# Optimization experiments

Measured on AMD Instinct MI355X. Metric: run time of the kernel, lower is better.

The kernel has to match this reference:

```python
import jax, jax.numpy as jnp
import numpy as np

N_NODES = 50000
N_EDGES = 800000
IN_CH = 128
OUT_CH = 64


def setup_inputs() -> dict:
    key = jax.random.key(0)
    ks = jax.random.split(key, 8)
    cat = IN_CH + OUT_CH
    scale = 1.0 / np.sqrt(cat)
    return {
        "x": jax.random.normal(ks[0], (N_NODES, IN_CH), dtype=jnp.float32),
        "edge_index": jax.random.randint(ks[1], (2, N_EDGES), 0, N_NODES, dtype=jnp.int64),
        "edge_weight": jax.random.uniform(ks[2], (N_EDGES,), dtype=jnp.float32),
        "hidden_state": jax.random.normal(ks[3], (N_NODES, OUT_CH), dtype=jnp.float32),
        "W_z": jax.random.normal(ks[4], (cat, OUT_CH), dtype=jnp.float32) * scale,
        "b_z": jnp.zeros((OUT_CH,), dtype=jnp.float32),
        "W_r": jax.random.normal(ks[5], (cat, OUT_CH), dtype=jnp.float32) * scale,
        "b_r": jnp.zeros((OUT_CH,), dtype=jnp.float32),
        "W_h": jax.random.normal(ks[6], (cat, OUT_CH), dtype=jnp.float32) * scale,
        "b_h": jnp.zeros((OUT_CH,), dtype=jnp.float32),
    }


def _gcn_norm(row, col, w, num_nodes):
    # PyG GCNConv normalization with self-loops (fill_value=1):
    # norm_e = deg[row]^-1/2 * w_e * deg[col]^-1/2 over loop-augmented edges
    loops = jnp.arange(num_nodes, dtype=row.dtype)
    row = jnp.concatenate([row, loops])
    col = jnp.concatenate([col, loops])
    w = jnp.concatenate([w, jnp.ones((num_nodes,), dtype=w.dtype)])
    deg = jax.ops.segment_sum(w, col, num_segments=num_nodes)
    dinv = jnp.where(deg > 0, jax.lax.rsqrt(deg), 0.0)
    norm = dinv[row] * w * dinv[col]
    return row, col, norm


def _gcn_conv(x_cat, W, b, row, col, norm, num_nodes):
    h = x_cat @ W                                   # (N, out)
    msg = h[row] * norm[:, None]                    # (E+N, out) gather + scale
    out = jax.ops.segment_sum(msg, col, num_segments=num_nodes)
    return out + b


def reference(x, edge_index, edge_weight, hidden_state,
              W_z, b_z, W_r, b_r, W_h, b_h):
    n = x.shape[0]
    row, col, norm = _gcn_norm(edge_index[0], edge_index[1], edge_weight, n)
    xh = jnp.concatenate([x, hidden_state], axis=1)
    z = jax.nn.sigmoid(_gcn_conv(xh, W_z, b_z, row, col, norm, n))
    r = jax.nn.sigmoid(_gcn_conv(xh, W_r, b_r, row, col, norm, n))
    xrh = jnp.concatenate([x, r * hidden_state], axis=1)
    h_cand = jnp.tanh(_gcn_conv(xrh, W_h, b_h, row, col, norm, n))
    return z * hidden_state + (1.0 - z) * h_cand
```

## Files before the change

### kernel.cpp

```cpp
#include <hip/hip_runtime.h>
#include <hip/hip_bf16.h>
#include <cstdint>
#include <cstddef>

#define IN_CH   128
#define OUT_CH  64
#define CAT_CH  192

typedef short bf16x8 __attribute__((ext_vector_type(8)));
typedef float f32x4  __attribute__((ext_vector_type(4)));
typedef unsigned long long u64;
typedef unsigned int u32;

__device__ __forceinline__ float sigmoidf_(float x) { return 1.f / (1.f + __expf(-x)); }

__device__ __forceinline__ unsigned short f2bf(float f) {
    u32 u = __float_as_uint(f);
    u32 r = (u + 0x7fffu + ((u >> 16) & 1u)) >> 16;
    return (unsigned short)r;
}
__device__ __forceinline__ float bflo(u32 v) { return __uint_as_float(v << 16); }
__device__ __forceinline__ float bfhi(u32 v) { return __uint_as_float(v & 0xffff0000u); }
__device__ __forceinline__ float bf1(unsigned short v) { return __uint_as_float((u32)v << 16); }

__global__ void detect_kernel(const unsigned int* __restrict__ ei, int* __restrict__ flag) {
    unsigned int v = ei[(threadIdx.x << 1) + 1];
    unsigned long long b = __ballot(v != 0u);
    if (threadIdx.x == 0) *flag = (b != 0ull) ? 1 : 0;
}

__device__ __forceinline__ int load_col(const void* ei, int i, int E, int f) {
    return f ? ((const int*)ei)[E + i] : (int)((const long long*)ei)[E + i];
}
__device__ __forceinline__ int load_row(const void* ei, int i, int E, int f) {
    return f ? ((const int*)ei)[i] : (int)((const long long*)ei)[i];
}

__global__ void hist2_kernel(const void* __restrict__ ei, const float* __restrict__ w,
                             u64* __restrict__ packed, u32* __restrict__ rank,
                             const int* __restrict__ flag, int E) {
    int i0 = (blockIdx.x * blockDim.x + threadIdx.x) * 4;
    if (i0 >= E) return;
    int f = *flag;
    u32 rk[4];
#pragma unroll
    for (int k = 0; k < 4; k++) {
        int i = i0 + k;
        if (i < E) {
            int c = load_col(ei, i, E, f);
            u32 wq = __float2uint_rn(w[i] * 1048576.0f);
            u64 old = atomicAdd(&packed[c], (1ull << 32) | (u64)wq);
            rk[k] = (u32)(old >> 32);
        }
    }
#pragma unroll
    for (int k = 0; k < 4; k++)
        if (i0 + k < E) rank[i0 + k] = rk[k];
}

__global__ void dinvc_kernel(const u64* __restrict__ packed, float* __restrict__ dinv,
                             int* __restrict__ counts, int n) {
    int i = blockIdx.x * blockDim.x + threadIdx.x;
    if (i >= n) return;
    u64 p = packed[i];
    float wsum = (float)(u32)(p & 0xffffffffull) * (1.0f / 1048576.0f);
    dinv[i] = rsqrtf(1.0f + wsum);
    counts[i] = (int)(p >> 32);
}

__global__ __launch_bounds__(256) void scan1_kernel(const int* __restrict__ counts,
                                                    int* __restrict__ starts,
                                                    int* __restrict__ bsum, int n) {
    __shared__ int s[256];
    int i = blockIdx.x * 256 + threadIdx.x;
    int v = (i < n) ? counts[i] : 0;
    s[threadIdx.x] = v;
    __syncthreads();
#pragma unroll
    for (int d = 1; d < 256; d <<= 1) {
        int t = (threadIdx.x >= d) ? s[threadIdx.x - d] : 0;
        __syncthreads();
        s[threadIdx.x] += t;
        __syncthreads();
    }
    if (i < n) starts[i] = s[threadIdx.x] - v;
    if (threadIdx.x == 255) bsum[blockIdx.x] = s[255];
}

__global__ __launch_bounds__(256) void scan2_kernel(int* __restrict__ bsum, int nb) {
    __shared__ int s[256];
    int t = threadIdx.x;
    int v = (t < nb) ? bsum[t] : 0;
    s[t] = v;
    __syncthreads();
#pragma unroll
    for (int d = 1; d < 256; d <<= 1) {
        int u = (t >= d) ? s[t - d] : 0;
        __syncthreads();
        s[t] += u;
        __syncthreads();
    }
    if (t < nb) bsum[t] = s[t] - v;
}

__global__ void scan3_kernel(int* __restrict__ starts, const int* __restrict__ boff,
                             int n, int E) {
    int i = blockIdx.x * blockDim.x + threadIdx.x;
    if (i == 0) starts[n] = E;
    if (i < n) starts[i] += boff[blockIdx.x];
}

__global__ void scatter2_kernel(const void* __restrict__ ei, const float* __restrict__ w,
                                const float* __restrict__ dinv, const int* __restrict__ starts,
                                const u32* __restrict__ rank, u64* __restrict__ pairs,
                                const int* __restrict__ flag, int E) {
    int i0 = (blockIdx.x * blockDim.x + threadIdx.x) * 4;
    if (i0 >= E) return;
    int f = *flag;
    int r[4], c[4];
#pragma unroll
    for (int k = 0; k < 4; k++) {
        int i = i0 + k;
        if (i < E) { r[k] = load_row(ei, i, E, f); c[k] = load_col(ei, i, E, f); }
    }
#pragma unroll
    for (int k = 0; k < 4; k++) {
        int i = i0 + k;
        if (i < E) {
            float nm = dinv[r[k]] * w[i] * dinv[c[k]];
            int pos = starts[c[k]] + (int)rank[i];
            pairs[pos] = ((u64)__float_as_uint(nm) << 32) | (u32)r[k];
        }
    }
}

__global__ void cvt_kernel(const float* __restrict__ x, const float* __restrict__ hidden,
                           unsigned short* __restrict__ xb, unsigned short* __restrict__ hb,
                           int nx, int nh) {
    int i4 = (blockIdx.x * blockDim.x + threadIdx.x) * 4;
    if (i4 < nx) {
        float4 v = *(const float4*)&x[i4];
        ushort4 o = { f2bf(v.x), f2bf(v.y), f2bf(v.z), f2bf(v.w) };
        *(ushort4*)&xb[i4] = o;
    } else {
        int j = i4 - nx;
        if (j < nh) {
            float4 v = *(const float4*)&hidden[j];
            ushort4 o = { f2bf(v.x), f2bf(v.y), f2bf(v.z), f2bf(v.w) };
            *(ushort4*)&hb[j] = o;
        }
    }
}

__global__ void packW_kernel(const float* __restrict__ Wz, const float* __restrict__ Wr,
                             const float* __restrict__ Wh,
                             unsigned short* __restrict__ Bzrt, unsigned short* __restrict__ Wht) {
    int i = blockIdx.x * blockDim.x + threadIdx.x;
    if (i >= 192 * CAT_CH) return;
    int col = i / CAT_CH, k = i % CAT_CH;
    if (col < 128) {
        float v = (col < 64) ? Wz[k * 64 + col] : Wr[k * 64 + (col - 64)];
        Bzrt[col * CAT_CH + k] = f2bf(v);
    } else {
        Wht[(col - 128) * CAT_CH + k] = f2bf(Wh[k * 64 + (col - 128)]);
    }
}

template <int TN>
__global__ __launch_bounds__(256) void gemm_bf16_kernel(
    const unsigned short* __restrict__ A0, int a0w,
    const unsigned short* __restrict__ A1, int a1w,
    const unsigned short* __restrict__ Bt,
    unsigned short* __restrict__ C, int nrows)
{
    __shared__ unsigned short As[128][48];
    __shared__ unsigned short Bs[TN][200];

    const int t = threadIdx.x, lane = t & 63, wave = t >> 6;
    const int rowBase = blockIdx.x * 128;

    for (int idx = t * 8; idx < TN * CAT_CH; idx += 256 * 8) {
        int col = idx / CAT_CH, k = idx % CAT_CH;
        *(int4*)&Bs[col][k] = *(const int4*)&Bt[idx];
    }

    f32x4 acc[2][TN / 16];
#pragma unroll
    for (int rf = 0; rf < 2; rf++)
#pragma unroll
        for (int cf = 0; cf < TN / 16; cf++) acc[rf][cf] = (f32x4){0.f, 0.f, 0.f, 0.f};

    const int srow = t >> 1, half = t & 1;
    int arow = rowBase + srow;
    if (arow >= nrows) arow = nrows - 1;

    for (int k0 = 0; k0 < CAT_CH; k0 += 32) {
        __syncthreads();
        {
            const unsigned short* src = (k0 < a0w)
                ? A0 + (size_t)arow * a0w + k0
                : A1 + (size_t)arow * a1w + (k0 - a0w);
            *(int4*)&As[srow][half * 16] = *(const int4*)(src + half * 16);
            *(int4*)&As[srow][half * 16 + 8] = *(const int4*)(src + half * 16 + 8);
        }
        __syncthreads();

        const int rbase = wave * 32;
        const int koff = (lane >> 4) * 8;
        bf16x8 a0 = *(const bf16x8*)&As[rbase + (lane & 15)][koff];
        bf16x8 a1 = *(const bf16x8*)&As[rbase + 16 + (lane & 15)][koff];
#pragma unroll
        for (int cf = 0; cf < TN / 16; cf++) {
            bf16x8 b = *(const bf16x8*)&Bs[cf * 16 + (lane & 15)][k0 + koff];
            acc[0][cf] = __builtin_amdgcn_mfma_f32_16x16x32_bf16(a0, b, acc[0][cf], 0, 0, 0);
            acc[1][cf] = __builtin_amdgcn_mfma_f32_16x16x32_bf16(a1, b, acc[1][cf], 0, 0, 0);
        }
    }

#pragma unroll
    for (int rf = 0; rf < 2; rf++)
#pragma unroll
        for (int cf = 0; cf < TN / 16; cf++) {
            int row0 = rowBase + wave * 32 + rf * 16 + (lane >> 4) * 4;
            int col  = cf * 16 + (lane & 15);
#pragma unroll
            for (int r = 0; r < 4; r++) {
                int row = row0 + r;
                if (row < nrows) C[(size_t)row * TN + col] = f2bf(acc[rf][cf][r]);
            }
        }
}

__global__ __launch_bounds__(256) void spmm_zr_kernel(
    const unsigned short* __restrict__ H, const u64* __restrict__ pairs,
    const int* __restrict__ starts, const float* __restrict__ dinv,
    const float* __restrict__ hidden, const float* __restrict__ bz,
    const float* __restrict__ br, float* __restrict__ Z,
    unsigned short* __restrict__ RHb, int N)
{
    int node = (blockIdx.x * 256 + threadIdx.x) >> 6;
    if (node >= N) return;
    int lane = threadIdx.x & 63;
    int s = starts[node], e = starts[node + 1];
    float d = dinv[node], d2 = d * d;
    const int ch = lane * 2;

    u32 self = *(const u32*)&H[(size_t)node * 128 + ch];
    float ax = bflo(self) * d2, ay = bfhi(self) * d2;

    for (int j = s; j < e; j += 8) {
        u32 hv[8]; float nm[8];
#pragma unroll
        for (int k = 0; k < 8; k++) {
            int jj = j + k;
            u64 p = pairs[(jj < e) ? jj : (e - 1)];
            nm[k] = (jj < e) ? __uint_as_float((u32)(p >> 32)) : 0.f;
            hv[k] = *(const u32*)&H[(size_t)(u32)p * 128 + ch];
        }
#pragma unroll
        for (int k = 0; k < 8; k++) {
            ax = fmaf(bflo(hv[k]), nm[k], ax);
            ay = fmaf(bfhi(hv[k]), nm[k], ay);
        }
    }

    if (lane < 32) {
        int c = ch;
        float2 o = { sigmoidf_(ax + bz[c]), sigmoidf_(ay + bz[c + 1]) };
        *(float2*)&Z[(size_t)node * 64 + c] = o;
    } else {
        int c = ch - 64;
        const float* hid = hidden + (size_t)node * 64 + c;
        float rh0 = sigmoidf_(ax + br[c])     * hid[0];
        float rh1 = sigmoidf_(ay + br[c + 1]) * hid[1];
        u32 packed = (u32)f2bf(rh0) | ((u32)f2bf(rh1) << 16);
        *(u32*)&RHb[(size_t)node * 64 + c] = packed;
    }
}

__global__ __launch_bounds__(256) void spmm_h_kernel(
    const unsigned short* __restrict__ H, const u64* __restrict__ pairs,
    const int* __restrict__ starts, const float* __restrict__ dinv,
    const float* __restrict__ hidden, const float* __restrict__ bh,
    const float* __restrict__ Z, float* __restrict__ out, int N)
{
    int node = (blockIdx.x * 256 + threadIdx.x) >> 6;
    if (node >= N) return;
    int lane = threadIdx.x & 63;
    int s = starts[node], e = starts[node + 1];
    float d = dinv[node], d2 = d * d;

    float acc = bf1(H[(size_t)node * 64 + lane]) * d2;

    for (int j = s; j < e; j += 8) {
        unsigned short hv[8]; float nm[8];
#pragma unroll
        for (int k = 0; k < 8; k++) {
            int jj = j + k;
            u64 p = pairs[(jj < e) ? jj : (e - 1)];
            nm[k] = (jj < e) ? __uint_as_float((u32)(p >> 32)) : 0.f;
            hv[k] = H[(size_t)(u32)p * 64 + lane];
        }
#pragma unroll
        for (int k = 0; k < 8; k++)
            acc = fmaf(bf1(hv[k]), nm[k], acc);
    }

    size_t idx = (size_t)node * 64 + lane;
    float hc = tanhf(acc + bh[lane]);
    float z  = Z[idx];
    out[idx] = z * hidden[idx] + (1.f - z) * hc;
}

extern "C" void kernel_launch(void* const* d_in, const int* in_sizes, int n_in,
                              void* d_out, int out_size, void* d_ws, size_t ws_size,
                              hipStream_t stream) {
    const float* x      = (const float*)d_in[0];
    const void*  eidx   = d_in[1];
    const float* ew     = (const float*)d_in[2];
    const float* hidden = (const float*)d_in[3];
    const float* Wz     = (const float*)d_in[4];
    const float* bz     = (const float*)d_in[5];
    const float* Wr     = (const float*)d_in[6];
    const float* br     = (const float*)d_in[7];
    const float* Wh     = (const float*)d_in[8];
    const float* bh     = (const float*)d_in[9];
    float* out = (float*)d_out;

    const int E = in_sizes[2];
    const int N = in_sizes[3] / OUT_CH;

    char* base = (char*)d_ws;
    size_t off = 0;
    auto carve = [&](size_t bytes) -> char* {
        char* p = base + off;
        off = (off + bytes + 255) & ~(size_t)255;
        return p;
    };
    u64*   packed = (u64*)  carve((size_t)N * 8);
    u32*   rank   = (u32*)  carve((size_t)E * 4);
    float* dinv   = (float*)carve((size_t)N * 4);
    int*   counts = (int*)  carve((size_t)N * 4);
    int*   starts = (int*)  carve((size_t)(N + 1) * 4);
    int*   bsum   = (int*)  carve(256 * 4);
    u64*   pairs  = (u64*)  carve((size_t)E * 8);
    unsigned short* xb   = (unsigned short*)carve((size_t)N * 128 * 2);
    unsigned short* hb   = (unsigned short*)carve((size_t)N * 64 * 2);
    unsigned short* Hzrb = (unsigned short*)carve((size_t)N * 128 * 2);
    unsigned short* RHb  = (unsigned short*)carve((size_t)N * 64 * 2);
    unsigned short* Hhb  = (unsigned short*)carve((size_t)N * 64 * 2);
    float* Z = (float*)carve((size_t)N * 64 * 4);
    unsigned short* Bzrt = (unsigned short*)carve((size_t)128 * CAT_CH * 2);
    unsigned short* Wht  = (unsigned short*)carve((size_t)64 * CAT_CH * 2);
    int* flag = (int*)carve(4);
    if (off > ws_size) return;

    const int B256 = 256;
    const int gE4 = (E + 1023) / 1024;
    const int gN = (N + B256 - 1) / B256;
    const int gM = (N + 127) / 128;
    const int gW = (N + 3) / 4;

    hipLaunchKernelGGL(detect_kernel, dim3(1), dim3(64), 0, stream,
                       (const unsigned int*)eidx, flag);

    hipMemsetAsync(packed, 0, (size_t)N * 8, stream);
    hipLaunchKernelGGL(hist2_kernel, dim3(gE4), dim3(B256), 0, stream,
                       eidx, ew, packed, rank, flag, E);
    hipLaunchKernelGGL(dinvc_kernel, dim3(gN), dim3(B256), 0, stream,
                       packed, dinv, counts, N);

    hipLaunchKernelGGL(scan1_kernel, dim3(gN), dim3(B256), 0, stream, counts, starts, bsum, N);
    hipLaunchKernelGGL(scan2_kernel, dim3(1), dim3(B256), 0, stream, bsum, gN);
    hipLaunchKernelGGL(scan3_kernel, dim3(gN), dim3(B256), 0, stream, starts, bsum, N, E);

    hipLaunchKernelGGL(scatter2_kernel, dim3(gE4), dim3(B256), 0, stream,
                       eidx, ew, dinv, starts, rank, pairs, flag, E);

    hipLaunchKernelGGL(cvt_kernel, dim3((N * CAT_CH / 4 + 255) / 256), dim3(B256), 0, stream,
                       x, hidden, xb, hb, N * 128, N * 64);
    hipLaunchKernelGGL(packW_kernel, dim3((192 * CAT_CH + 255) / 256), dim3(B256), 0, stream,
                       Wz, Wr, Wh, Bzrt, Wht);

    hipLaunchKernelGGL((gemm_bf16_kernel<128>), dim3(gM), dim3(B256), 0, stream,
                       xb, 128, hb, 64, Bzrt, Hzrb, N);

    hipLaunchKernelGGL(spmm_zr_kernel, dim3(gW), dim3(B256), 0, stream,
                       Hzrb, pairs, starts, dinv, hidden, bz, br, Z, RHb, N);

    hipLaunchKernelGGL((gemm_bf16_kernel<64>), dim3(gM), dim3(B256), 0, stream,
                       xb, 128, RHb, 64, Wht, Hhb, N);

    hipLaunchKernelGGL(spmm_h_kernel, dim3(gW), dim3(B256), 0, stream,
                       Hhb, pairs, starts, dinv, hidden, bh, Z, out, N);
}
```

Baseline: 202.8 us.

## Chunk GEMM outputs into 16-column slabs and split SpMM gathers per chunk

The GEMM now writes its bf16 output in a column-chunked layout, with each 16-channel slab stored contiguously across all nodes. The SpMM kernels assign a block to one chunk, so the gathered rows come from a much smaller working set that fits better in L2. Each wave splits a node's edges across 8 lane groups of 8 lanes and combines the partial sums with shuffles. The dinv computation is also folded into the first scan kernel, removing one launch and the counts buffer. The cost is that edge indices (pairs) are now re-read once per chunk, 8 times for z/r and 4 for h, and that launches more blocks.

```diff
diff --git a/kernel.cpp b/kernel.cpp
--- a/kernel.cpp
+++ b/kernel.cpp
@@ -21,7 +21,6 @@
 }
 __device__ __forceinline__ float bflo(u32 v) { return __uint_as_float(v << 16); }
 __device__ __forceinline__ float bfhi(u32 v) { return __uint_as_float(v & 0xffff0000u); }
-__device__ __forceinline__ float bf1(unsigned short v) { return __uint_as_float((u32)v << 16); }
 
 __global__ void detect_kernel(const unsigned int* __restrict__ ei, int* __restrict__ flag) {
     unsigned int v = ei[(threadIdx.x << 1) + 1];
@@ -58,22 +57,19 @@
         if (i0 + k < E) rank[i0 + k] = rk[k];
 }
 
-__global__ void dinvc_kernel(const u64* __restrict__ packed, float* __restrict__ dinv,
-                             int* __restrict__ counts, int n) {
-    int i = blockIdx.x * blockDim.x + threadIdx.x;
-    if (i >= n) return;
-    u64 p = packed[i];
-    float wsum = (float)(u32)(p & 0xffffffffull) * (1.0f / 1048576.0f);
-    dinv[i] = rsqrtf(1.0f + wsum);
-    counts[i] = (int)(p >> 32);
-}
-
-__global__ __launch_bounds__(256) void scan1_kernel(const int* __restrict__ counts,
+__global__ __launch_bounds__(256) void scan1_kernel(const u64* __restrict__ packed,
+                                                    float* __restrict__ dinv,
                                                     int* __restrict__ starts,
                                                     int* __restrict__ bsum, int n) {
     __shared__ int s[256];
     int i = blockIdx.x * 256 + threadIdx.x;
-    int v = (i < n) ? counts[i] : 0;
+    int v = 0;
+    if (i < n) {
+        u64 p = packed[i];
+        float wsum = (float)(u32)(p & 0xffffffffull) * (1.0f / 1048576.0f);
+        dinv[i] = rsqrtf(1.0f + wsum);
+        v = (int)(p >> 32);
+    }
     s[threadIdx.x] = v;
     __syncthreads();
 #pragma unroll
@@ -222,13 +218,41 @@
 #pragma unroll
         for (int cf = 0; cf < TN / 16; cf++) {
             int row0 = rowBase + wave * 32 + rf * 16 + (lane >> 4) * 4;
-            int col  = cf * 16 + (lane & 15);
 #pragma unroll
             for (int r = 0; r < 4; r++) {
                 int row = row0 + r;
-                if (row < nrows) C[(size_t)row * TN + col] = f2bf(acc[rf][cf][r]);
+                if (row < nrows)
+                    C[((size_t)cf * nrows + row) * 16 + (lane & 15)] = f2bf(acc[rf][cf][r]);
             }
         }
+}
+
+__device__ __forceinline__ float2 gather_acc(
+    const unsigned short* __restrict__ Hp, const u64* __restrict__ pairs,
+    int s, int e, int oct, int sub, float ax, float ay)
+{
+    for (int j = s; j < e; j += 16) {
+        u32 hv[2]; float nm[2];
+#pragma unroll
+        for (int k = 0; k < 2; k++) {
+            int jj = j + k * 8 + oct;
+            int jc = (jj < e) ? jj : (e - 1);
+            u64 p = pairs[jc];
+            nm[k] = (jj < e) ? __uint_as_float((u32)(p >> 32)) : 0.f;
+            hv[k] = *(const u32*)&Hp[(size_t)(u32)p * 16 + sub * 2];
+        }
+#pragma unroll
+        for (int k = 0; k < 2; k++) {
+            ax = fmaf(bflo(hv[k]), nm[k], ax);
+            ay = fmaf(bfhi(hv[k]), nm[k], ay);
+        }
+    }
+#pragma unroll
+    for (int d = 8; d <= 32; d <<= 1) {
+        ax += __shfl_xor(ax, d, 64);
+        ay += __shfl_xor(ay, d, 64);
+    }
+    return make_float2(ax, ay);
 }
 
 __global__ __launch_bounds__(256) void spmm_zr_kernel(
@@ -238,43 +262,33 @@
     const float* __restrict__ br, float* __restrict__ Z,
     unsigned short* __restrict__ RHb, int N)
 {
-    int node = (blockIdx.x * 256 + threadIdx.x) >> 6;
+    int bid = blockIdx.x;
+    int ck  = bid & 7;
+    int node = (bid >> 3) * 4 + (threadIdx.x >> 6);
     if (node >= N) return;
-    int lane = threadIdx.x & 63;
+    int lane = threadIdx.x & 63, oct = lane >> 3, sub = lane & 7;
+
+    const unsigned short* Hp = H + (size_t)ck * N * 16;
     int s = starts[node], e = starts[node + 1];
     float d = dinv[node], d2 = d * d;
-    const int ch = lane * 2;
-
-    u32 self = *(const u32*)&H[(size_t)node * 128 + ch];
-    float ax = bflo(self) * d2, ay = bfhi(self) * d2;
-
-    for (int j = s; j < e; j += 8) {
-        u32 hv[8]; float nm[8];
-#pragma unroll
-        for (int k = 0; k < 8; k++) {
-            int jj = j + k;
-            u64 p = pairs[(jj < e) ? jj : (e - 1)];
-            nm[k] = (jj < e) ? __uint_as_float((u32)(p >> 32)) : 0.f;
-            hv[k] = *(const u32*)&H[(size_t)(u32)p * 128 + ch];
-        }
-#pragma unroll
-        for (int k = 0; k < 8; k++) {
-            ax = fmaf(bflo(hv[k]), nm[k], ax);
-            ay = fmaf(bfhi(hv[k]), nm[k], ay);
-        }
-    }
-
-    if (lane < 32) {
-        int c = ch;
-        float2 o = { sigmoidf_(ax + bz[c]), sigmoidf_(ay + bz[c + 1]) };
-        *(float2*)&Z[(size_t)node * 64 + c] = o;
-    } else {
-        int c = ch - 64;
-        const float* hid = hidden + (size_t)node * 64 + c;
-        float rh0 = sigmoidf_(ax + br[c])     * hid[0];
-        float rh1 = sigmoidf_(ay + br[c + 1]) * hid[1];
-        u32 packed = (u32)f2bf(rh0) | ((u32)f2bf(rh1) << 16);
-        *(u32*)&RHb[(size_t)node * 64 + c] = packed;
+
+    u32 self = *(const u32*)&Hp[(size_t)node * 16 + sub * 2];
+    float ax = (oct == 0) ? bflo(self) * d2 : 0.f;
+    float ay = (oct == 0) ? bfhi(self) * d2 : 0.f;
+    float2 a = gather_acc(Hp, pairs, s, e, oct, sub, ax, ay);
+
+    if (oct == 0) {
+        if (ck < 4) {
+            int c = ck * 16 + sub * 2;
+            float2 o = { sigmoidf_(a.x + bz[c]), sigmoidf_(a.y + bz[c + 1]) };
+            *(float2*)&Z[(size_t)node * 64 + c] = o;
+        } else {
+            int c = (ck - 4) * 16 + sub * 2;
+            const float* hid = hidden + (size_t)node * 64 + c;
+            float rh0 = sigmoidf_(a.x + br[c])     * hid[0];
+            float rh1 = sigmoidf_(a.y + br[c + 1]) * hid[1];
+            *(u32*)&RHb[(size_t)node * 64 + c] = (u32)f2bf(rh0) | ((u32)f2bf(rh1) << 16);
+        }
     }
 }
 
@@ -284,32 +298,33 @@
     const float* __restrict__ hidden, const float* __restrict__ bh,
     const float* __restrict__ Z, float* __restrict__ out, int N)
 {
-    int node = (blockIdx.x * 256 + threadIdx.x) >> 6;
+    int bid = blockIdx.x;
+    int slot = bid & 7;
+    int ck = slot & 3, halfg = slot >> 2;
+    int node = (bid >> 3) * 8 + halfg * 4 + (threadIdx.x >> 6);
     if (node >= N) return;
-    int lane = threadIdx.x & 63;
+    int lane = threadIdx.x & 63, oct = lane >> 3, sub = lane & 7;
+
+    const unsigned short* Hp = H + (size_t)ck * N * 16;
     int s = starts[node], e = starts[node + 1];
     float d = dinv[node], d2 = d * d;
 
-    float acc = bf1(H[(size_t)node * 64 + lane]) * d2;
-
-    for (int j = s; j < e; j += 8) {
-        unsigned short hv[8]; float nm[8];
-#pragma unroll
-        for (int k = 0; k < 8; k++) {
-            int jj = j + k;
-            u64 p = pairs[(jj < e) ? jj : (e - 1)];
-            nm[k] = (jj < e) ? __uint_as_float((u32)(p >> 32)) : 0.f;
-            hv[k] = H[(size_t)(u32)p * 64 + lane];
-        }
-#pragma unroll
-        for (int k = 0; k < 8; k++)
-            acc = fmaf(bf1(hv[k]), nm[k], acc);
-    }
-
-    size_t idx = (size_t)node * 64 + lane;
-    float hc = tanhf(acc + bh[lane]);
-    float z  = Z[idx];
-    out[idx] = z * hidden[idx] + (1.f - z) * hc;
+    u32 self = *(const u32*)&Hp[(size_t)node * 16 + sub * 2];
+    float ax = (oct == 0) ? bflo(self) * d2 : 0.f;
+    float ay = (oct == 0) ? bfhi(self) * d2 : 0.f;
+    float2 a = gather_acc(Hp, pairs, s, e, oct, sub, ax, ay);
+
+    if (oct == 0) {
+        int c = ck * 16 + sub * 2;
+        size_t idx = (size_t)node * 64 + c;
+        float2 hid = *(const float2*)&hidden[idx];
+        float2 z   = *(const float2*)&Z[idx];
+        float hc0 = tanhf(a.x + bh[c]);
+        float hc1 = tanhf(a.y + bh[c + 1]);
+        float2 o = { z.x * hid.x + (1.f - z.x) * hc0,
+                     z.y * hid.y + (1.f - z.y) * hc1 };
+        *(float2*)&out[idx] = o;
+    }
 }
 
 extern "C" void kernel_launch(void* const* d_in, const int* in_sizes, int n_in,
@@ -340,7 +355,6 @@
     u64*   packed = (u64*)  carve((size_t)N * 8);
     u32*   rank   = (u32*)  carve((size_t)E * 4);
     float* dinv   = (float*)carve((size_t)N * 4);
-    int*   counts = (int*)  carve((size_t)N * 4);
     int*   starts = (int*)  carve((size_t)(N + 1) * 4);
     int*   bsum   = (int*)  carve(256 * 4);
     u64*   pairs  = (u64*)  carve((size_t)E * 8);
@@ -359,7 +373,8 @@
     const int gE4 = (E + 1023) / 1024;
     const int gN = (N + B256 - 1) / B256;
     const int gM = (N + 127) / 128;
-    const int gW = (N + 3) / 4;
+    const int gZR = ((N + 3) / 4) * 8;
+    const int gH  = ((N + 7) / 8) * 8;
 
     hipLaunchKernelGGL(detect_kernel, dim3(1), dim3(64), 0, stream,
                        (const unsigned int*)eidx, flag);
@@ -367,10 +382,9 @@
     hipMemsetAsync(packed, 0, (size_t)N * 8, stream);
     hipLaunchKernelGGL(hist2_kernel, dim3(gE4), dim3(B256), 0, stream,
                        eidx, ew, packed, rank, flag, E);
-    hipLaunchKernelGGL(dinvc_kernel, dim3(gN), dim3(B256), 0, stream,
-                       packed, dinv, counts, N);
-
-    hipLaunchKernelGGL(scan1_kernel, dim3(gN), dim3(B256), 0, stream, counts, starts, bsum, N);
+
+    hipLaunchKernelGGL(scan1_kernel, dim3(gN), dim3(B256), 0, stream,
+                       packed, dinv, starts, bsum, N);
     hipLaunchKernelGGL(scan2_kernel, dim3(1), dim3(B256), 0, stream, bsum, gN);
     hipLaunchKernelGGL(scan3_kernel, dim3(gN), dim3(B256), 0, stream, starts, bsum, N, E);
 
@@ -385,12 +399,12 @@
     hipLaunchKernelGGL((gemm_bf16_kernel<128>), dim3(gM), dim3(B256), 0, stream,
                        xb, 128, hb, 64, Bzrt, Hzrb, N);
 
-    hipLaunchKernelGGL(spmm_zr_kernel, dim3(gW), dim3(B256), 0, stream,
+    hipLaunchKernelGGL(spmm_zr_kernel, dim3(gZR), dim3(B256), 0, stream,
                        Hzrb, pairs, starts, dinv, hidden, bz, br, Z, RHb, N);
 
     hipLaunchKernelGGL((gemm_bf16_kernel<64>), dim3(gM), dim3(B256), 0, stream,
                        xb, 128, RHb, 64, Wht, Hhb, N);
 
-    hipLaunchKernelGGL(spmm_h_kernel, dim3(gW), dim3(B256), 0, stream,
+    hipLaunchKernelGGL(spmm_h_kernel, dim3(gH), dim3(B256), 0, stream,
                        Hhb, pairs, starts, dinv, hidden, bh, Z, out, N);
 }
```

New measurement: 305.2 us. +50.5%, slower.
